# Kernel optimization log

Measured on AMD Instinct MI355X. Metric: run time of the kernel, lower is better.

## Reference

```python
import jax, jax.numpy as jnp
import numpy as np

H = 256       # hidden_dim
E = H // 2    # operator embedding dim
T = 12        # num_tempers
O = 3         # num_ops per temper
HOPS = 4      # max_path_hops
B = 128       # batch
D = 2048      # input_dim
NCLS = 10     # task_head classes


def setup_inputs() -> dict:
    key = jax.random.key(0)
    ks = jax.random.split(key, 12)
    x = jax.random.normal(ks[0], (B, D), jnp.float32)
    N = B * (D // H)  # 1024 patch tokens
    # per-hop routed temper per patch; value == T means halt
    sampled_tempers = jax.random.randint(ks[1], (HOPS, N), 0, T + 1, jnp.int32)
    sampled_ops = jax.random.randint(ks[2], (HOPS, N), 0, O, jnp.int32)
    s1 = 1.0 / np.sqrt(H + E)
    W1 = jax.random.uniform(ks[3], (T, O, H + E, H), jnp.float32, -s1, s1)
    b1 = jax.random.uniform(ks[4], (T, O, H), jnp.float32, -s1, s1)
    s2 = 1.0 / np.sqrt(H)
    W2 = jax.random.uniform(ks[5], (T, O, H, H), jnp.float32, -s2, s2)
    b2 = jax.random.uniform(ks[6], (T, O, H), jnp.float32, -s2, s2)
    op_emb = jax.random.normal(ks[7], (T, O, E), jnp.float32)
    ln_g = jnp.ones((H,), jnp.float32)
    ln_b = jnp.zeros((H,), jnp.float32)
    Wt = jax.random.uniform(ks[8], (H, NCLS), jnp.float32, -s2, s2)
    bt = jax.random.uniform(ks[9], (NCLS,), jnp.float32, -s2, s2)
    return dict(x=x, W1=W1, b1=b1, W2=W2, b2=b2, op_emb=op_emb,
                ln_g=ln_g, ln_b=ln_b, Wt=Wt, bt=bt,
                sampled_tempers=sampled_tempers, sampled_ops=sampled_ops)


def reference(x, W1, b1, W2, b2, op_emb, ln_g, ln_b, Wt, bt,
              sampled_tempers, sampled_ops):
    Bsz, Din = x.shape
    pad = (-Din) % H
    if pad > 0:
        x = jnp.pad(x, ((0, 0), (0, pad)))
    state = x.reshape(-1, H)                       # [N, H] patch states
    active = jnp.ones((state.shape[0],), bool)     # not-yet-halted mask
    for hop in range(HOPS):
        t = sampled_tempers[hop]
        o = sampled_ops[hop]
        active = active & (t != T)                 # T == halt action
        tc = jnp.clip(t, 0, T - 1)                 # safe index for halted rows
        emb = op_emb[tc, o]                        # [N, E] op embedding gather
        xa = jnp.concatenate([state, emb], axis=-1)  # [N, H+E]
        # per-token expert weight gather + batched matvec (memory-bound dispatch)
        h = jax.nn.relu(jnp.einsum('ni,nio->no', xa, W1[tc, o]) + b1[tc, o])
        y = jax.nn.relu(jnp.einsum('ni,nio->no', h, W2[tc, o]) + b2[tc, o])
        state = jnp.where(active[:, None], y, state)
    pooled = state.reshape(Bsz, -1, H).mean(axis=1)   # [B, H]
    mu = pooled.mean(axis=-1, keepdims=True)
    var = pooled.var(axis=-1, keepdims=True)
    normed = (pooled - mu) * jax.lax.rsqrt(var + 1e-5) * ln_g + ln_b
    return normed @ Wt + bt                           # [B, 10]
```

## Files before the change

### kernel.cpp

```cpp
#include <hip/hip_runtime.h>

typedef __attribute__((ext_vector_type(8))) short short8;
typedef __attribute__((ext_vector_type(4))) float floatx4;

#define NEXP   36
#define NTOK   1024
#define HOPS   4

#define OFF_STATE   0u
#define OFF_W1B     1048576u
#define OFF_W2B     5767168u
#define OFF_C1      10485760u
#define OFF_COUNTS  10522624u
#define OFF_LISTS   10523264u
#define OFF_VER     11113088u

__device__ __forceinline__ unsigned short f2bf(float f) {
    unsigned u = __float_as_uint(f);
    u += 0x7FFFu + ((u >> 16) & 1u);
    return (unsigned short)(u >> 16);
}

__global__ __launch_bounds__(256) void prep_kernel(
    const float* __restrict__ W1, const float* __restrict__ b1,
    const float* __restrict__ W2, const float* __restrict__ op_emb,
    const int* __restrict__ tempers, const int* __restrict__ ops,
    unsigned short* __restrict__ W1b, unsigned short* __restrict__ W2b,
    float* __restrict__ c1, int* __restrict__ counts, int* __restrict__ lists,
    int* __restrict__ ver)
{
    const int bid = blockIdx.x;
    const int t = threadIdx.x;

    if (bid < 2880) {
        const int r  = bid & 7;
        const int q  = bid >> 3;
        const int e  = r + 8 * (q >> 6);
        if (e >= NEXP) return;
        const int sub = q & 63;
        const int mat = sub >> 5;
        const int s2  = sub & 31;
        const int kb  = s2 >> 2;
        const int jt  = s2 & 3;
        const float* src = mat ? (W2 + e * 65536) : (W1 + e * 98304);
        unsigned short* dst = (mat ? W2b : W1b) + e * 65536;
        const int j  = jt * 64 + (t & 63);
        const int ks = (t >> 6) * 8;
        short8 v;
        #pragma unroll
        for (int i = 0; i < 8; i++)
            v[i] = (short)f2bf(src[(kb * 32 + ks + i) * 256 + j]);
        *(short8*)(dst + (kb * 256 + j) * 32 + ks) = v;
    } else if (bid < 2916) {
        const int e = bid - 2880;
        __shared__ float eb[128];
        if (t < 128) eb[t] = op_emb[e * 128 + t];
        __syncthreads();
        float acc = b1[e * 256 + t];
        const float* wp = W1 + e * 98304 + 65536;
        #pragma unroll 4
        for (int k = 0; k < 128; k++)
            acc += eb[k] * wp[k * 256 + t];
        c1[e * 256 + t] = acc;
    } else {
        __shared__ int lc[HOPS * NEXP];
        if (t < HOPS * NEXP) lc[t] = 0;
        for (int i = t; i < NTOK; i += 256) ver[i] = 0;
        __syncthreads();
        for (int q = 0; q < 4; q++) {
            int n = q * 256 + t;
            bool act = true;
            for (int hop = 0; hop < HOPS; hop++) {
                int tt = tempers[hop * NTOK + n];
                int oo = ops[hop * NTOK + n];
                act = act && (tt != 12);
                if (act) {
                    int e = tt * 3 + oo;
                    int pos = atomicAdd(&lc[hop * NEXP + e], 1);
                    lists[(hop * NEXP + e) * NTOK + pos] = n;
                }
            }
        }
        __syncthreads();
        if (t < HOPS * NEXP) counts[t] = lc[t];
    }
}

__global__ __launch_bounds__(1024, 4) void mega_hop_kernel(
    const float* __restrict__ x, float* __restrict__ state,
    const unsigned short* __restrict__ W1b,
    const unsigned short* __restrict__ W2b,
    const float* __restrict__ c1, const float* __restrict__ b2,
    const int* __restrict__ counts, const int* __restrict__ lists,
    int* __restrict__ ver)
{
    const int e    = blockIdx.x % 40;
    const int slot = blockIdx.x / 40;
    if (e >= NEXP) return;

    int ne[HOPS];
    bool any = false;
    #pragma unroll
    for (int h = 0; h < HOPS; h++) {
        ne[h] = counts[h * NEXP + e];
        any = any || (slot * 16 < ne[h]);
    }
    if (!any) return;

    const int t = threadIdx.x;
    const int l = t & 63, w = t >> 6;
    const int col = l & 15, g = l >> 4;
    const int j = w * 16 + col;

    const unsigned short* Wp  = W1b + e * 65536;
    const unsigned short* Wp2 = W2b + e * 65536;
    short8 B1[8], B2[8];
    #pragma unroll
    for (int kb = 0; kb < 8; kb++) {
        B1[kb] = *(const short8*)(Wp  + (kb * 256 + j) * 32 + g * 8);
        B2[kb] = *(const short8*)(Wp2 + (kb * 256 + j) * 32 + g * 8);
    }
    #pragma unroll
    for (int kb = 0; kb < 8; kb++) {
        asm volatile("" : "+v"(B1[kb]));
        asm volatile("" : "+v"(B2[kb]));
    }
    const float cv = c1[e * 256 + j];
    const float bv = b2[e * 256 + j];

    __shared__ int toks[16];
    __shared__ unsigned short Ab[4096];
    __shared__ unsigned short Hb[4096];

    for (int hop = 0; hop < HOPS; hop++) {
        const float* src = hop ? state : x;
        for (int m0 = slot * 16; m0 < ne[hop]; m0 += 64) {
            const int mact = min(16, ne[hop] - m0);
            __syncthreads();
            if (t < 16) {
                int tok = (t < mact)
                        ? lists[(hop * NEXP + e) * NTOK + m0 + t] : -1;
                toks[t] = tok;
                if (hop > 0 && tok >= 0) {
                    while (__hip_atomic_load(&ver[tok], __ATOMIC_RELAXED,
                                             __HIP_MEMORY_SCOPE_AGENT) < hop)
                        __builtin_amdgcn_s_sleep(1);
                    (void)__hip_atomic_load(&ver[tok], __ATOMIC_ACQUIRE,
                                            __HIP_MEMORY_SCOPE_AGENT);
                }
            }
            __syncthreads();

            {
                int m = t >> 6;
                int k = (t & 63) * 4;
                float4 v = make_float4(0.f, 0.f, 0.f, 0.f);
                if (m < mact) v = *(const float4*)(src + toks[m] * 256 + k);
                int kb = k >> 5, gg = (k >> 3) & 3, i = k & 7;
                unsigned short* d = Ab + kb * 512 + (gg * 16 + m) * 8 + i;
                d[0] = f2bf(v.x); d[1] = f2bf(v.y);
                d[2] = f2bf(v.z); d[3] = f2bf(v.w);
            }
            __syncthreads();

            floatx4 acc = (floatx4){cv, cv, cv, cv};
            #pragma unroll
            for (int kb = 0; kb < 8; kb++) {
                short8 a = *(const short8*)(Ab + kb * 512 + l * 8);
                acc = __builtin_amdgcn_mfma_f32_16x16x32_bf16(a, B1[kb], acc, 0, 0, 0);
            }
            {
                int kb2 = j >> 5, g2 = (j >> 3) & 3, i2 = j & 7;
                #pragma unroll
                for (int r = 0; r < 4; r++) {
                    int m = g * 4 + r;
                    float vv = acc[r];
                    vv = vv > 0.f ? vv : 0.f;
                    Hb[kb2 * 512 + (g2 * 16 + m) * 8 + i2] = f2bf(vv);
                }
            }
            __syncthreads();

            floatx4 acc2 = (floatx4){bv, bv, bv, bv};
            #pragma unroll
            for (int kb = 0; kb < 8; kb++) {
                short8 a = *(const short8*)(Hb + kb * 512 + l * 8);
                acc2 = __builtin_amdgcn_mfma_f32_16x16x32_bf16(a, B2[kb], acc2, 0, 0, 0);
            }
            #pragma unroll
            for (int r = 0; r < 4; r++) {
                int m = g * 4 + r;
                if (m < mact) {
                    float vv = acc2[r];
                    state[toks[m] * 256 + j] = vv > 0.f ? vv : 0.f;
                }
            }

            if (hop < HOPS - 1) {
                __syncthreads();
                if (t == 0) __threadfence();
                __syncthreads();
                if (t < mact)
                    __hip_atomic_fetch_add(&ver[toks[t]], 1, __ATOMIC_RELEASE,
                                           __HIP_MEMORY_SCOPE_AGENT);
            }
        }
    }
}

__global__ __launch_bounds__(256) void final_kernel(
    const float* __restrict__ x, const float* __restrict__ state,
    const int* __restrict__ tempers,
    const float* __restrict__ ln_g, const float* __restrict__ ln_b,
    const float* __restrict__ Wt, const float* __restrict__ bt,
    float* __restrict__ out)
{
    const int b = blockIdx.x, t = threadIdx.x;
    float s = 0.f;
    #pragma unroll
    for (int p = 0; p < 8; p++) {
        int n = b * 8 + p;
        const float* rowsrc = (tempers[n] != 12) ? state : x;
        s += rowsrc[n * 256 + t];
    }
    s *= 0.125f;

    float v1 = s, v2 = s * s;
    #pragma unroll
    for (int off = 32; off; off >>= 1) {
        v1 += __shfl_down(v1, off);
        v2 += __shfl_down(v2, off);
    }
    __shared__ float red[8];
    __shared__ float stats[2];
    const int w = t >> 6, l = t & 63;
    if (l == 0) { red[w] = v1; red[4 + w] = v2; }
    __syncthreads();
    if (t == 0) {
        float su = red[0] + red[1] + red[2] + red[3];
        float sq = red[4] + red[5] + red[6] + red[7];
        float mu = su * (1.0f / 256.0f);
        float var = sq * (1.0f / 256.0f) - mu * mu;
        stats[0] = mu;
        stats[1] = rsqrtf(var + 1e-5f);
    }
    __syncthreads();
    float normed = (s - stats[0]) * stats[1] * ln_g[t] + ln_b[t];

    __shared__ float pr[40];
    #pragma unroll
    for (int c = 0; c < 10; c++) {
        float pv = normed * Wt[t * 10 + c];
        #pragma unroll
        for (int off = 32; off; off >>= 1) pv += __shfl_down(pv, off);
        if (l == 0) pr[w * 10 + c] = pv;
    }
    __syncthreads();
    if (t < 10)
        out[b * 10 + t] = pr[t] + pr[10 + t] + pr[20 + t] + pr[30 + t] + bt[t];
}

extern "C" void kernel_launch(void* const* d_in, const int* in_sizes, int n_in,
                              void* d_out, int out_size, void* d_ws, size_t ws_size,
                              hipStream_t stream)
{
    const float* x      = (const float*)d_in[0];
    const float* W1     = (const float*)d_in[1];
    const float* b1     = (const float*)d_in[2];
    const float* W2     = (const float*)d_in[3];
    const float* b2     = (const float*)d_in[4];
    const float* op_emb = (const float*)d_in[5];
    const float* ln_g   = (const float*)d_in[6];
    const float* ln_b   = (const float*)d_in[7];
    const float* Wt     = (const float*)d_in[8];
    const float* bt     = (const float*)d_in[9];
    const int* tempers  = (const int*)d_in[10];
    const int* ops      = (const int*)d_in[11];

    char* ws = (char*)d_ws;
    float* state          = (float*)(ws + OFF_STATE);
    unsigned short* W1b   = (unsigned short*)(ws + OFF_W1B);
    unsigned short* W2b   = (unsigned short*)(ws + OFF_W2B);
    float* c1             = (float*)(ws + OFF_C1);
    int* counts           = (int*)(ws + OFF_COUNTS);
    int* lists            = (int*)(ws + OFF_LISTS);
    int* ver              = (int*)(ws + OFF_VER);
    float* out            = (float*)d_out;

    prep_kernel<<<2917, 256, 0, stream>>>(W1, b1, W2, op_emb, tempers, ops,
                                          W1b, W2b, c1, counts, lists, ver);
    mega_hop_kernel<<<160, 1024, 0, stream>>>(x, state, W1b, W2b, c1, b2,
                                              counts, lists, ver);
    final_kernel<<<128, 256, 0, stream>>>(x, state, tempers,
                                          ln_g, ln_b, Wt, bt, out);
}
```

Baseline: 135.4 us.

## Fuse final pooling/LayerNorm/head into hop kernel via global completion counter

Merges the final pooling, LayerNorm and classifier stage into the persistent hop kernel. Every block bumps a global done counter when it finishes, and the first 128 blocks spin until all 160 have arrived before computing the output, which removes one kernel launch and its gap. The prep kernel is also reordered so the token-list build and embedding-bias blocks get the lowest block IDs, which should make counts ready sooner relative to the weight conversion blocks. This relies on all 160 blocks being co-resident, since a grid-wide spin barrier could deadlock otherwise.

```diff
diff --git a/kernel.cpp b/kernel.cpp
--- a/kernel.cpp
+++ b/kernel.cpp
@@ -6,6 +6,7 @@
 #define NEXP   36
 #define NTOK   1024
 #define HOPS   4
+#define NMEGA  160
 
 #define OFF_STATE   0u
 #define OFF_W1B     1048576u
@@ -14,6 +15,7 @@
 #define OFF_COUNTS  10522624u
 #define OFF_LISTS   10523264u
 #define OFF_VER     11113088u
+#define OFF_DONE    11117184u
 
 __device__ __forceinline__ unsigned short f2bf(float f) {
     unsigned u = __float_as_uint(f);
@@ -27,14 +29,48 @@
     const int* __restrict__ tempers, const int* __restrict__ ops,
     unsigned short* __restrict__ W1b, unsigned short* __restrict__ W2b,
     float* __restrict__ c1, int* __restrict__ counts, int* __restrict__ lists,
-    int* __restrict__ ver)
+    int* __restrict__ ver, int* __restrict__ done)
 {
     const int bid = blockIdx.x;
     const int t = threadIdx.x;
 
-    if (bid < 2880) {
-        const int r  = bid & 7;
-        const int q  = bid >> 3;
+    if (bid == 0) {
+        __shared__ int lc[HOPS * NEXP];
+        if (t < HOPS * NEXP) lc[t] = 0;
+        for (int i = t; i < NTOK; i += 256) ver[i] = 0;
+        if (t == 0) *done = 0;
+        __syncthreads();
+        for (int q = 0; q < 4; q++) {
+            int n = q * 256 + t;
+            bool act = true;
+            for (int hop = 0; hop < HOPS; hop++) {
+                int tt = tempers[hop * NTOK + n];
+                int oo = ops[hop * NTOK + n];
+                act = act && (tt != 12);
+                if (act) {
+                    int e = tt * 3 + oo;
+                    int pos = atomicAdd(&lc[hop * NEXP + e], 1);
+                    lists[(hop * NEXP + e) * NTOK + pos] = n;
+                }
+            }
+        }
+        __syncthreads();
+        if (t < HOPS * NEXP) counts[t] = lc[t];
+    } else if (bid < 37) {
+        const int e = bid - 1;
+        __shared__ float eb[128];
+        if (t < 128) eb[t] = op_emb[e * 128 + t];
+        __syncthreads();
+        float acc = b1[e * 256 + t];
+        const float* wp = W1 + e * 98304 + 65536;
+        #pragma unroll 4
+        for (int k = 0; k < 128; k++)
+            acc += eb[k] * wp[k * 256 + t];
+        c1[e * 256 + t] = acc;
+    } else if (bid >= 40) {
+        const int bb = bid - 40;
+        const int r  = bb & 7;
+        const int q  = bb >> 3;
         const int e  = r + 8 * (q >> 6);
         if (e >= NEXP) return;
         const int sub = q & 63;
@@ -51,213 +87,208 @@
         for (int i = 0; i < 8; i++)
             v[i] = (short)f2bf(src[(kb * 32 + ks + i) * 256 + j]);
         *(short8*)(dst + (kb * 256 + j) * 32 + ks) = v;
-    } else if (bid < 2916) {
-        const int e = bid - 2880;
-        __shared__ float eb[128];
-        if (t < 128) eb[t] = op_emb[e * 128 + t];
-        __syncthreads();
-        float acc = b1[e * 256 + t];
-        const float* wp = W1 + e * 98304 + 65536;
-        #pragma unroll 4
-        for (int k = 0; k < 128; k++)
-            acc += eb[k] * wp[k * 256 + t];
-        c1[e * 256 + t] = acc;
-    } else {
-        __shared__ int lc[HOPS * NEXP];
-        if (t < HOPS * NEXP) lc[t] = 0;
-        for (int i = t; i < NTOK; i += 256) ver[i] = 0;
-        __syncthreads();
-        for (int q = 0; q < 4; q++) {
-            int n = q * 256 + t;
-            bool act = true;
-            for (int hop = 0; hop < HOPS; hop++) {
-                int tt = tempers[hop * NTOK + n];
-                int oo = ops[hop * NTOK + n];
-                act = act && (tt != 12);
-                if (act) {
-                    int e = tt * 3 + oo;
-                    int pos = atomicAdd(&lc[hop * NEXP + e], 1);
-                    lists[(hop * NEXP + e) * NTOK + pos] = n;
-                }
-            }
-        }
-        __syncthreads();
-        if (t < HOPS * NEXP) counts[t] = lc[t];
     }
 }
 
-__global__ __launch_bounds__(1024, 4) void mega_hop_kernel(
+__global__ __launch_bounds__(1024, 4) void mega_kernel(
     const float* __restrict__ x, float* __restrict__ state,
     const unsigned short* __restrict__ W1b,
     const unsigned short* __restrict__ W2b,
     const float* __restrict__ c1, const float* __restrict__ b2,
     const int* __restrict__ counts, const int* __restrict__ lists,
-    int* __restrict__ ver)
-{
-    const int e    = blockIdx.x % 40;
-    const int slot = blockIdx.x / 40;
-    if (e >= NEXP) return;
-
-    int ne[HOPS];
-    bool any = false;
-    #pragma unroll
-    for (int h = 0; h < HOPS; h++) {
-        ne[h] = counts[h * NEXP + e];
-        any = any || (slot * 16 < ne[h]);
-    }
-    if (!any) return;
-
-    const int t = threadIdx.x;
-    const int l = t & 63, w = t >> 6;
-    const int col = l & 15, g = l >> 4;
-    const int j = w * 16 + col;
-
-    const unsigned short* Wp  = W1b + e * 65536;
-    const unsigned short* Wp2 = W2b + e * 65536;
-    short8 B1[8], B2[8];
-    #pragma unroll
-    for (int kb = 0; kb < 8; kb++) {
-        B1[kb] = *(const short8*)(Wp  + (kb * 256 + j) * 32 + g * 8);
-        B2[kb] = *(const short8*)(Wp2 + (kb * 256 + j) * 32 + g * 8);
-    }
-    #pragma unroll
-    for (int kb = 0; kb < 8; kb++) {
-        asm volatile("" : "+v"(B1[kb]));
-        asm volatile("" : "+v"(B2[kb]));
-    }
-    const float cv = c1[e * 256 + j];
-    const float bv = b2[e * 256 + j];
-
-    __shared__ int toks[16];
-    __shared__ unsigned short Ab[4096];
-    __shared__ unsigned short Hb[4096];
-
-    for (int hop = 0; hop < HOPS; hop++) {
-        const float* src = hop ? state : x;
-        for (int m0 = slot * 16; m0 < ne[hop]; m0 += 64) {
-            const int mact = min(16, ne[hop] - m0);
-            __syncthreads();
-            if (t < 16) {
-                int tok = (t < mact)
-                        ? lists[(hop * NEXP + e) * NTOK + m0 + t] : -1;
-                toks[t] = tok;
-                if (hop > 0 && tok >= 0) {
-                    while (__hip_atomic_load(&ver[tok], __ATOMIC_RELAXED,
-                                             __HIP_MEMORY_SCOPE_AGENT) < hop)
-                        __builtin_amdgcn_s_sleep(1);
-                    (void)__hip_atomic_load(&ver[tok], __ATOMIC_ACQUIRE,
-                                            __HIP_MEMORY_SCOPE_AGENT);
-                }
-            }
-            __syncthreads();
-
-            {
-                int m = t >> 6;
-                int k = (t & 63) * 4;
-                float4 v = make_float4(0.f, 0.f, 0.f, 0.f);
-                if (m < mact) v = *(const float4*)(src + toks[m] * 256 + k);
-                int kb = k >> 5, gg = (k >> 3) & 3, i = k & 7;
-                unsigned short* d = Ab + kb * 512 + (gg * 16 + m) * 8 + i;
-                d[0] = f2bf(v.x); d[1] = f2bf(v.y);
-                d[2] = f2bf(v.z); d[3] = f2bf(v.w);
-            }
-            __syncthreads();
-
-            floatx4 acc = (floatx4){cv, cv, cv, cv};
-            #pragma unroll
-            for (int kb = 0; kb < 8; kb++) {
-                short8 a = *(const short8*)(Ab + kb * 512 + l * 8);
-                acc = __builtin_amdgcn_mfma_f32_16x16x32_bf16(a, B1[kb], acc, 0, 0, 0);
-            }
-            {
-                int kb2 = j >> 5, g2 = (j >> 3) & 3, i2 = j & 7;
-                #pragma unroll
-                for (int r = 0; r < 4; r++) {
-                    int m = g * 4 + r;
-                    float vv = acc[r];
-                    vv = vv > 0.f ? vv : 0.f;
-                    Hb[kb2 * 512 + (g2 * 16 + m) * 8 + i2] = f2bf(vv);
-                }
-            }
-            __syncthreads();
-
-            floatx4 acc2 = (floatx4){bv, bv, bv, bv};
-            #pragma unroll
-            for (int kb = 0; kb < 8; kb++) {
-                short8 a = *(const short8*)(Hb + kb * 512 + l * 8);
-                acc2 = __builtin_amdgcn_mfma_f32_16x16x32_bf16(a, B2[kb], acc2, 0, 0, 0);
-            }
-            #pragma unroll
-            for (int r = 0; r < 4; r++) {
-                int m = g * 4 + r;
-                if (m < mact) {
-                    float vv = acc2[r];
-                    state[toks[m] * 256 + j] = vv > 0.f ? vv : 0.f;
-                }
-            }
-
-            if (hop < HOPS - 1) {
-                __syncthreads();
-                if (t == 0) __threadfence();
-                __syncthreads();
-                if (t < mact)
-                    __hip_atomic_fetch_add(&ver[toks[t]], 1, __ATOMIC_RELEASE,
-                                           __HIP_MEMORY_SCOPE_AGENT);
-            }
-        }
-    }
-}
-
-__global__ __launch_bounds__(256) void final_kernel(
-    const float* __restrict__ x, const float* __restrict__ state,
+    int* __restrict__ ver, int* __restrict__ done,
     const int* __restrict__ tempers,
     const float* __restrict__ ln_g, const float* __restrict__ ln_b,
     const float* __restrict__ Wt, const float* __restrict__ bt,
     float* __restrict__ out)
 {
-    const int b = blockIdx.x, t = threadIdx.x;
-    float s = 0.f;
-    #pragma unroll
-    for (int p = 0; p < 8; p++) {
-        int n = b * 8 + p;
-        const float* rowsrc = (tempers[n] != 12) ? state : x;
-        s += rowsrc[n * 256 + t];
-    }
-    s *= 0.125f;
-
-    float v1 = s, v2 = s * s;
-    #pragma unroll
-    for (int off = 32; off; off >>= 1) {
-        v1 += __shfl_down(v1, off);
-        v2 += __shfl_down(v2, off);
-    }
+    const int bid  = blockIdx.x;
+    const int e    = bid % 40;
+    const int slot = bid / 40;
+    const int t    = threadIdx.x;
+    const int l = t & 63, w = t >> 6;
+    const int col = l & 15, g = l >> 4;
+    const int j = w * 16 + col;
+
+    __shared__ int toks[16];
+    __shared__ unsigned short Ab[4096];
+    __shared__ unsigned short Hb[4096];
+    __shared__ float pool[4][256];
     __shared__ float red[8];
     __shared__ float stats[2];
-    const int w = t >> 6, l = t & 63;
-    if (l == 0) { red[w] = v1; red[4 + w] = v2; }
+    __shared__ float pr[40];
+
+    int ne[HOPS];
+    bool work = false;
+    if (e < NEXP) {
+        #pragma unroll
+        for (int h = 0; h < HOPS; h++) {
+            ne[h] = counts[h * NEXP + e];
+            work = work || (slot * 16 < ne[h]);
+        }
+    }
+
+    if (work) {
+        const unsigned short* Wp  = W1b + e * 65536;
+        const unsigned short* Wp2 = W2b + e * 65536;
+        short8 B1[8], B2[8];
+        #pragma unroll
+        for (int kb = 0; kb < 8; kb++) {
+            B1[kb] = *(const short8*)(Wp  + (kb * 256 + j) * 32 + g * 8);
+            B2[kb] = *(const short8*)(Wp2 + (kb * 256 + j) * 32 + g * 8);
+        }
+        #pragma unroll
+        for (int kb = 0; kb < 8; kb++) {
+            asm volatile("" : "+v"(B1[kb]));
+            asm volatile("" : "+v"(B2[kb]));
+        }
+        const float cv = c1[e * 256 + j];
+        const float bv = b2[e * 256 + j];
+
+        for (int hop = 0; hop < HOPS; hop++) {
+            const float* src = hop ? state : x;
+            for (int m0 = slot * 16; m0 < ne[hop]; m0 += 64) {
+                const int mact = min(16, ne[hop] - m0);
+                __syncthreads();
+                if (t < 16) {
+                    int tok = (t < mact)
+                            ? lists[(hop * NEXP + e) * NTOK + m0 + t] : -1;
+                    toks[t] = tok;
+                    if (hop > 0 && tok >= 0) {
+                        while (__hip_atomic_load(&ver[tok], __ATOMIC_RELAXED,
+                                                 __HIP_MEMORY_SCOPE_AGENT) < hop)
+                            __builtin_amdgcn_s_sleep(1);
+                        (void)__hip_atomic_load(&ver[tok], __ATOMIC_ACQUIRE,
+                                                __HIP_MEMORY_SCOPE_AGENT);
+                    }
+                }
+                __syncthreads();
+
+                {
+                    int m = t >> 6;
+                    int k = (t & 63) * 4;
+                    float4 v = make_float4(0.f, 0.f, 0.f, 0.f);
+                    if (m < mact) v = *(const float4*)(src + toks[m] * 256 + k);
+                    int kb = k >> 5, gg = (k >> 3) & 3, i = k & 7;
+                    unsigned short* d = Ab + kb * 512 + (gg * 16 + m) * 8 + i;
+                    d[0] = f2bf(v.x); d[1] = f2bf(v.y);
+                    d[2] = f2bf(v.z); d[3] = f2bf(v.w);
+                }
+                __syncthreads();
+
+                floatx4 acc = (floatx4){cv, cv, cv, cv};
+                #pragma unroll
+                for (int kb = 0; kb < 8; kb++) {
+                    short8 a = *(const short8*)(Ab + kb * 512 + l * 8);
+                    acc = __builtin_amdgcn_mfma_f32_16x16x32_bf16(a, B1[kb], acc, 0, 0, 0);
+                }
+                {
+                    int kb2 = j >> 5, g2 = (j >> 3) & 3, i2 = j & 7;
+                    #pragma unroll
+                    for (int r = 0; r < 4; r++) {
+                        int m = g * 4 + r;
+                        float vv = acc[r];
+                        vv = vv > 0.f ? vv : 0.f;
+                        Hb[kb2 * 512 + (g2 * 16 + m) * 8 + i2] = f2bf(vv);
+                    }
+                }
+                __syncthreads();
+
+                floatx4 acc2 = (floatx4){bv, bv, bv, bv};
+                #pragma unroll
+                for (int kb = 0; kb < 8; kb++) {
+                    short8 a = *(const short8*)(Hb + kb * 512 + l * 8);
+                    acc2 = __builtin_amdgcn_mfma_f32_16x16x32_bf16(a, B2[kb], acc2, 0, 0, 0);
+                }
+                #pragma unroll
+                for (int r = 0; r < 4; r++) {
+                    int m = g * 4 + r;
+                    if (m < mact) {
+                        float vv = acc2[r];
+                        state[toks[m] * 256 + j] = vv > 0.f ? vv : 0.f;
+                    }
+                }
+
+                if (hop < HOPS - 1) {
+                    __syncthreads();
+                    if (t == 0) __threadfence();
+                    __syncthreads();
+                    if (t < mact)
+                        __hip_atomic_fetch_add(&ver[toks[t]], 1,
+                                               __ATOMIC_RELEASE,
+                                               __HIP_MEMORY_SCOPE_AGENT);
+                }
+            }
+        }
+    }
+
     __syncthreads();
     if (t == 0) {
-        float su = red[0] + red[1] + red[2] + red[3];
-        float sq = red[4] + red[5] + red[6] + red[7];
-        float mu = su * (1.0f / 256.0f);
-        float var = sq * (1.0f / 256.0f) - mu * mu;
-        stats[0] = mu;
-        stats[1] = rsqrtf(var + 1e-5f);
-    }
-    __syncthreads();
-    float normed = (s - stats[0]) * stats[1] * ln_g[t] + ln_b[t];
-
-    __shared__ float pr[40];
-    #pragma unroll
-    for (int c = 0; c < 10; c++) {
-        float pv = normed * Wt[t * 10 + c];
-        #pragma unroll
-        for (int off = 32; off; off >>= 1) pv += __shfl_down(pv, off);
-        if (l == 0) pr[w * 10 + c] = pv;
-    }
-    __syncthreads();
-    if (t < 10)
-        out[b * 10 + t] = pr[t] + pr[10 + t] + pr[20 + t] + pr[30 + t] + bt[t];
+        __threadfence();
+        __hip_atomic_fetch_add(done, 1, __ATOMIC_RELEASE,
+                               __HIP_MEMORY_SCOPE_AGENT);
+    }
+
+    if (bid < 128) {
+        if (t == 0) {
+            while (__hip_atomic_load(done, __ATOMIC_RELAXED,
+                                     __HIP_MEMORY_SCOPE_AGENT) < NMEGA)
+                __builtin_amdgcn_s_sleep(2);
+            (void)__hip_atomic_load(done, __ATOMIC_ACQUIRE,
+                                    __HIP_MEMORY_SCOPE_AGENT);
+        }
+        __syncthreads();
+
+        const int b = bid;
+        {
+            const int c = t & 255, grp = t >> 8;
+            float s = 0.f;
+            #pragma unroll
+            for (int pp = 0; pp < 2; pp++) {
+                int n = b * 8 + grp * 2 + pp;
+                const float* rowsrc = (tempers[n] != 12) ? state : x;
+                s += rowsrc[n * 256 + c];
+            }
+            pool[grp][c] = s;
+        }
+        __syncthreads();
+        float pooled = 0.f;
+        if (t < 256) {
+            pooled = (pool[0][t] + pool[1][t] + pool[2][t] + pool[3][t]) * 0.125f;
+            float v1 = pooled, v2 = pooled * pooled;
+            #pragma unroll
+            for (int off = 32; off; off >>= 1) {
+                v1 += __shfl_down(v1, off);
+                v2 += __shfl_down(v2, off);
+            }
+            const int wq = t >> 6, lq = t & 63;
+            if (lq == 0) { red[wq] = v1; red[4 + wq] = v2; }
+        }
+        __syncthreads();
+        if (t == 0) {
+            float su = red[0] + red[1] + red[2] + red[3];
+            float sq = red[4] + red[5] + red[6] + red[7];
+            float mu = su * (1.0f / 256.0f);
+            float var = sq * (1.0f / 256.0f) - mu * mu;
+            stats[0] = mu;
+            stats[1] = rsqrtf(var + 1e-5f);
+        }
+        __syncthreads();
+        if (t < 256) {
+            float normed = (pooled - stats[0]) * stats[1] * ln_g[t] + ln_b[t];
+            const int wq = t >> 6, lq = t & 63;
+            #pragma unroll
+            for (int c = 0; c < 10; c++) {
+                float pv = normed * Wt[t * 10 + c];
+                #pragma unroll
+                for (int off = 32; off; off >>= 1) pv += __shfl_down(pv, off);
+                if (lq == 0) pr[wq * 10 + c] = pv;
+            }
+        }
+        __syncthreads();
+        if (t < 10)
+            out[b * 10 + t] = pr[t] + pr[10 + t] + pr[20 + t] + pr[30 + t] + bt[t];
+    }
 }
 
 extern "C" void kernel_launch(void* const* d_in, const int* in_sizes, int n_in,
@@ -285,12 +316,13 @@
     int* counts           = (int*)(ws + OFF_COUNTS);
     int* lists            = (int*)(ws + OFF_LISTS);
     int* ver              = (int*)(ws + OFF_VER);
+    int* done             = (int*)(ws + OFF_DONE);
     float* out            = (float*)d_out;
 
-    prep_kernel<<<2917, 256, 0, stream>>>(W1, b1, W2, op_emb, tempers, ops,
-                                          W1b, W2b, c1, counts, lists, ver);
-    mega_hop_kernel<<<160, 1024, 0, stream>>>(x, state, W1b, W2b, c1, b2,
-                                              counts, lists, ver);
-    final_kernel<<<128, 256, 0, stream>>>(x, state, tempers,
-                                          ln_g, ln_b, Wt, bt, out);
+    prep_kernel<<<2920, 256, 0, stream>>>(W1, b1, W2, op_emb, tempers, ops,
+                                          W1b, W2b, c1, counts, lists,
+                                          ver, done);
+    mega_kernel<<<NMEGA, 1024, 0, stream>>>(x, state, W1b, W2b, c1, b2,
+                                            counts, lists, ver, done,
+                                            tempers, ln_g, ln_b, Wt, bt, out);
 }
```

Result: slower. 145.6 us (+7.5%).
